# Kernel optimization log

Hardware: AMD Instinct MI355X
Metric: run time of the kernel (lower is better)

Reference implementation:

```python
import jax, jax.numpy as jnp
import numpy as np

B, N, P = 256, 32, 32
OBS, ACT = 96, 32
OBS_P, ACT_P = 96, 32
DIN = OBS + ACT          # obs_act_input_dim = 128
DOUT = 128               # obs_act_output_dim
DIN_P = OBS_P + ACT_P    # obs_act_input_dim_people = 128
DOUT_P = 128             # obs_act_output_dim_people
DF1, DF2 = 64, 32        # final hidden / final_output_dim


def setup_inputs() -> dict:
    key = jax.random.key(0)
    ks = jax.random.split(key, 13)
    s = 0.05
    return {
        "states": jax.random.normal(ks[0], (B, N, OBS), jnp.float32),
        "policies": jax.random.uniform(ks[1], (B, N, ACT), jnp.float32),
        "actions": jax.random.uniform(ks[2], (B, N, ACT), jnp.float32),
        "states_people": jax.random.normal(ks[3], (B, P, OBS_P), jnp.float32),
        "actions_people": jax.random.uniform(ks[4], (B, P, ACT_P), jnp.float32),
        "W_k": jax.random.normal(ks[5], (DIN, DOUT), jnp.float32) * s,
        "W_q": jax.random.normal(ks[6], (DIN, DOUT), jnp.float32) * s,
        "W_v": jax.random.normal(ks[7], (DIN, DOUT), jnp.float32) * s,
        "W_kp": jax.random.normal(ks[8], (DIN_P, DOUT_P), jnp.float32) * s,
        "W_qp": jax.random.normal(ks[9], (DIN, DOUT), jnp.float32) * s,
        "W_vp": jax.random.normal(ks[10], (DIN_P, DOUT_P), jnp.float32) * s,
        "W_f1": jax.random.normal(ks[11], (DOUT + DOUT_P, DF1), jnp.float32) * s,
        "W_f2": jax.random.normal(ks[12], (DF1, DF2), jnp.float32) * s,
    }


def reference(states, policies, actions, states_people, actions_people,
              W_k, W_q, W_v, W_kp, W_qp, W_vp, W_f1, W_f2):
    n = states.shape[1]
    p = states_people.shape[1]
    dk = jnp.asarray(W_k.shape[1], states.dtype)
    dkp = jnp.asarray(W_kp.shape[1], states.dtype)

    oa = jnp.concatenate([states, actions], axis=-1)    # [B,N,DIN]
    op = jnp.concatenate([states, policies], axis=-1)   # [B,N,DIN]

    k = oa @ W_k   # [B,N,DOUT]
    q = oa @ W_q   # [B,N,DOUT]
    scores = jnp.einsum('bid,bjd->bij', q, k)            # [B,N,N]
    # torch path: transpose then softmax over last axis of transposed scores
    weight = jax.nn.softmax(jnp.swapaxes(scores, 1, 2) / jnp.sqrt(dk), axis=-1)  # [B,N,N]

    # place_policies/place_actions masks == identity selector over (i==j)
    eye = jnp.eye(n, dtype=oa.dtype)[None, :, :, None]   # [1,N,N,1]
    oap = eye * op[:, None, :, :] + (1.0 - eye) * oa[:, None, :, :]  # [B,N,N,DIN]
    av = jnp.tanh(oap @ W_v)                             # [B,N,N,DOUT]
    # torch: mean_j( av[b,i,j] * weight[b,a,j] ) -> [B,N(a),N(i),DOUT]
    wav = jnp.einsum('baj,bijd->baid', weight, av) / n

    oa_p = jnp.concatenate([states_people, actions_people], axis=-1)  # [B,P,DIN_P]
    kp = oa_p @ W_kp                                     # [B,P,DOUT_P]
    qp = oa @ W_qp                                       # [B,N,DOUT_P]
    avp = jnp.tanh(oa_p @ W_vp)                          # [B,P,DOUT_P]
    scores_p = jnp.einsum('bnd,bpd->bnp', qp, kp)        # [B,N,P]
    # original softmax over dim=-2 (agents)
    wp = jax.nn.softmax(scores_p / jnp.sqrt(dkp), axis=-2)           # [B,N,P]
    wavp = jnp.einsum('bnp,bpd->bnd', wp, avp) / p       # mean over people

    wavp_b = jnp.broadcast_to(wavp[:, :, None, :], wav.shape[:3] + (wavp.shape[-1],))
    node_features = jnp.concatenate([wav, wavp_b], axis=-1)          # [B,N,N,256]

    h = jax.nn.leaky_relu(node_features @ W_f1)          # slope 0.01 (torch default)
    value = h @ W_f2                                     # [B,N,N,DF2]
    return value, weight, wp[..., None]
```

## Files before the change

kernel.cpp:

```cpp
#include <hip/hip_runtime.h>

#define VAL_SZ  (256*32*32*32)
#define W_OFF   VAL_SZ
#define WP_OFF  (VAL_SZ + 256*32*32)

#define PK_WV   0
#define PK_WVP  16384
#define PK_WQ   32768
#define PK_WK   49152
#define PK_WQP  65536
#define PK_WKP  81920
#define PK_WF1  98304
#define PK_WF2  114688

typedef short  bf16x8 __attribute__((ext_vector_type(8)));
typedef float  f32x4  __attribute__((ext_vector_type(4)));

#define MFMA(a, b, c) __builtin_amdgcn_mfma_f32_16x16x32_bf16(a, b, c, 0, 0, 0)

static __device__ __forceinline__ unsigned short f2bf(float f) {
    union { float f; unsigned u; } v; v.f = f;
    unsigned r = (v.u + 0x7FFF + ((v.u >> 16) & 1)) >> 16;
    return (unsigned short)r;
}
static __device__ __forceinline__ float bf2f(unsigned short u) {
    union { unsigned u; float f; } v; v.u = ((unsigned)u) << 16;
    return v.f;
}
static __device__ __forceinline__ float fast_tanh(float x) {
    x = fminf(fmaxf(x, -12.0f), 12.0f);
    float e = __expf(2.0f * x);
    return (e - 1.0f) / (e + 1.0f);
}

static __device__ __forceinline__ bf16x8 afrag(const unsigned short* Mb, int stride,
                                               int row0, int kt) {
    int lane = threadIdx.x & 63;
    return *(const bf16x8*)(Mb + (row0 + (lane & 15)) * stride + kt * 32 + (lane >> 4) * 8);
}

static __device__ __forceinline__ bf16x8 bfrag_pk(const unsigned short* base, int NT,
                                                  int kt, int nt) {
    int lane = threadIdx.x & 63;
    return *(const bf16x8*)(base + (((kt * NT + nt) * 64) + lane) * 8);
}

__global__ __launch_bounds__(256) void pack_lite(
    const float* __restrict__ Wk, const float* __restrict__ Wq,
    const float* __restrict__ Wv, const float* __restrict__ Wkp,
    const float* __restrict__ Wqp, const float* __restrict__ Wvp,
    const float* __restrict__ Wf1, const float* __restrict__ Wf2,
    unsigned short* __restrict__ pk)
{
    const float scale = 0.08838834764831845f;
    int gid = blockIdx.x * 256 + threadIdx.x;
    if (gid >= 14592) return;

    const float* W; int off, NT, ldn; float s = 1.0f;
    int r;
    if (gid < 12288) {
        int mat = gid >> 11;
        r = gid & 2047;
        NT = 8; ldn = 128;
        switch (mat) {
            case 0: W = Wv;  off = PK_WV;  break;
            case 1: W = Wvp; off = PK_WVP; break;
            case 2: W = Wq;  off = PK_WQ;  s = scale; break;
            case 3: W = Wk;  off = PK_WK;  break;
            case 4: W = Wqp; off = PK_WQP; s = scale; break;
            default: W = Wkp; off = PK_WKP; break;
        }
    } else if (gid < 14336) {
        r = gid - 12288; W = Wf1; off = PK_WF1; NT = 4; ldn = 64;
    } else {
        r = gid - 14336; W = Wf2; off = PK_WF2; NT = 2; ldn = 32;
    }
    int lane = r & 63;
    int l16 = lane & 15, quad = lane >> 4;
    int ktnt = r >> 6;
    int nt = ktnt % NT, kt = ktnt / NT;
    int n = nt * 16 + l16;
    int kb = kt * 32 + quad * 8;
    union { unsigned short u[8]; bf16x8 v; } o;
#pragma unroll
    for (int j = 0; j < 8; ++j) o.u[j] = f2bf(W[(kb + j) * ldn + n] * s);
    *(bf16x8*)(pk + off + (ktnt * 64 + lane) * 8) = o.v;
}

__global__ __launch_bounds__(1024) void critic_fused(
    const float* __restrict__ states, const float* __restrict__ policies,
    const float* __restrict__ actions, const float* __restrict__ states_p,
    const float* __restrict__ actions_p,
    const unsigned short* __restrict__ pk, float* __restrict__ out)
{
    __shared__ __align__(16) unsigned char SM[64000];
    unsigned short* OA  = (unsigned short*)(SM + 0);
    unsigned short* TD  = (unsigned short*)(SM + 8704);
    unsigned short* NF  = (unsigned short*)(SM + 0);
    unsigned short* OP  = (unsigned short*)(SM + 17408);
    unsigned short* QL  = (unsigned short*)(SM + 26112);
    unsigned short* WPB = (unsigned short*)(SM + 26112);
    float*          FP  = (float*)(SM + 26112);
    unsigned short* KL  = (unsigned short*)(SM + 34816);
    float*          GP  = (float*)(SM + 34816);
    unsigned short* VT  = (unsigned short*)(SM + 43520);
    unsigned short* AVT = (unsigned short*)(SM + 51712);
    unsigned short* SB1 = (unsigned short*)(SM + 59904);
    unsigned short* SB2 = (unsigned short*)(SM + 61952);

    const int tid = threadIdx.x;
    const int b = blockIdx.x;
    const int lane = tid & 63, wv = tid >> 6;
    const int l16 = lane & 15, quad = lane >> 4;
    const float invN = 1.0f / 32.0f;
    const f32x4 Z = {0.f, 0.f, 0.f, 0.f};

    {
        const float* st = states   + (size_t)b * 3072;
        const float* ac = actions  + (size_t)b * 1024;
        const float* po = policies + (size_t)b * 1024;
#pragma unroll
        for (int k = 0; k < 4; ++k) {
            int idx = tid + k * 1024;
            int n = idx >> 7, d = idx & 127;
            float sv, pv;
            if (d < 96) { sv = st[n * 96 + d]; pv = sv; }
            else        { sv = ac[n * 32 + d - 96]; pv = po[n * 32 + d - 96]; }
            OA[n * 136 + d] = f2bf(sv);
            OP[n * 136 + d] = f2bf(pv);
        }
    }
    __syncthreads();

    if (wv < 8) {
        int mt = wv & 1, ntA = wv >> 1, ntB = ntA + 4;
        f32x4 va0 = Z, va1 = Z, vp0 = Z, vp1 = Z;
#pragma unroll
        for (int kt = 0; kt < 4; ++kt) {
            bf16x8 aA = afrag(OA, 136, mt * 16, kt);
            bf16x8 aP = afrag(OP, 136, mt * 16, kt);
            bf16x8 b0 = bfrag_pk(pk + PK_WV, 8, kt, ntA);
            bf16x8 b1 = bfrag_pk(pk + PK_WV, 8, kt, ntB);
            va0 = MFMA(aA, b0, va0); va1 = MFMA(aA, b1, va1);
            vp0 = MFMA(aP, b0, vp0); vp1 = MFMA(aP, b1, vp1);
        }
#pragma unroll
        for (int r = 0; r < 4; ++r) {
            int row = mt * 16 + quad * 4 + r;
            float tva0 = fast_tanh(va0[r]), tvp0 = fast_tanh(vp0[r]);
            float tva1 = fast_tanh(va1[r]), tvp1 = fast_tanh(vp1[r]);
            VT[(ntA * 16 + l16) * 32 + row] = f2bf(tva0);
            VT[(ntB * 16 + l16) * 32 + row] = f2bf(tva1);
            TD[row * 136 + ntA * 16 + l16] = f2bf(tvp0 - tva0);
            TD[row * 136 + ntB * 16 + l16] = f2bf(tvp1 - tva1);
        }
    } else {
        int s = wv - 8;
        int mt = s & 1, pb2 = s >> 1;
        bf16x8 afr[4];
#pragma unroll
        for (int kt = 0; kt < 4; ++kt) afr[kt] = afrag(OA, 136, mt * 16, kt);
#pragma unroll
        for (int m2 = 0; m2 < 2; ++m2) {
            const unsigned short* pkM = pk + (m2 ? PK_WK : PK_WQ);
            unsigned short* dst = m2 ? KL : QL;
#pragma unroll
            for (int h = 0; h < 2; ++h) {
                int nt = pb2 + h * 4;
                f32x4 acc = Z;
#pragma unroll
                for (int kt = 0; kt < 4; ++kt)
                    acc = MFMA(afr[kt], bfrag_pk(pkM, 8, kt, nt), acc);
#pragma unroll
                for (int r = 0; r < 4; ++r)
                    dst[(mt * 16 + quad * 4 + r) * 136 + nt * 16 + l16] = f2bf(acc[r]);
            }
        }
    }
    __syncthreads();

    f32x4 gReg = Z;
    int gmt = 0, gnt = 0;
    if (wv < 8) {
        gmt = wv & 1; gnt = wv >> 1;
#pragma unroll
        for (int kt = 0; kt < 4; ++kt)
            gReg = MFMA(afrag(TD, 136, gmt * 16, kt), bfrag_pk(pk + PK_WF1, 4, kt, gnt), gReg);
    } else if (wv < 12) {
        int s = wv - 8;
        int mt = s & 1, nt = s >> 1;
        f32x4 acc = Z;
#pragma unroll
        for (int kt = 0; kt < 4; ++kt)
            acc = MFMA(afrag(QL, 136, mt * 16, kt), afrag(KL, 136, nt * 16, kt), acc);
#pragma unroll
        for (int r = 0; r < 4; ++r)
            SB1[(nt * 16 + l16) * 32 + mt * 16 + quad * 4 + r] = f2bf(acc[r]);
    } else {
        const float* st = states_p  + (size_t)b * 3072;
        const float* ac = actions_p + (size_t)b * 1024;
        int t256 = tid - 768;
#pragma unroll
        for (int k = 0; k < 16; ++k) {
            int idx = t256 + k * 256;
            int n = idx >> 7, d = idx & 127;
            OP[n * 136 + d] = f2bf((d < 96) ? st[n * 96 + d] : ac[n * 32 + d - 96]);
        }
    }
    __syncthreads();

    {
        int mt = wv & 1, nt = wv >> 1;
        bf16x8 ao[4], ap[4];
#pragma unroll
        for (int kt = 0; kt < 4; ++kt) {
            ao[kt] = afrag(OA, 136, mt * 16, kt);
            ap[kt] = afrag(OP, 136, mt * 16, kt);
        }
        f32x4 aq = Z, akp = Z, aav = Z;
#pragma unroll
        for (int kt = 0; kt < 4; ++kt) {
            aq  = MFMA(ao[kt], bfrag_pk(pk + PK_WQP, 8, kt, nt), aq);
            akp = MFMA(ap[kt], bfrag_pk(pk + PK_WKP, 8, kt, nt), akp);
            aav = MFMA(ap[kt], bfrag_pk(pk + PK_WVP, 8, kt, nt), aav);
        }
#pragma unroll
        for (int r = 0; r < 4; ++r) {
            int row = mt * 16 + quad * 4 + r;
            QL[row * 136 + nt * 16 + l16] = f2bf(aq[r]);
            KL[row * 136 + nt * 16 + l16] = f2bf(akp[r]);
            AVT[(nt * 16 + l16) * 32 + row] = f2bf(fast_tanh(aav[r]));
        }
    }
    __syncthreads();

    if (wv < 4) {
        int mt = wv & 1, nt = wv >> 1;
        f32x4 acc = Z;
#pragma unroll
        for (int kt = 0; kt < 4; ++kt)
            acc = MFMA(afrag(QL, 136, mt * 16, kt), afrag(KL, 136, nt * 16, kt), acc);
#pragma unroll
        for (int r = 0; r < 4; ++r)
            SB2[(nt * 16 + l16) * 32 + mt * 16 + quad * 4 + r] = f2bf(acc[r]);
    } else if (wv >= 8) {
        int t512 = tid - 512;
#pragma unroll
        for (int rep = 0; rep < 2; ++rep) {
            int idx = t512 + rep * 512;
            int j = idx & 31, a = idx >> 5;
            float x = bf2f(SB1[a * 32 + j]);
            float m = x;
#pragma unroll
            for (int msk = 16; msk >= 1; msk >>= 1) m = fmaxf(m, __shfl_xor(m, msk));
            float e = __expf(x - m);
            float s = e;
#pragma unroll
            for (int msk = 16; msk >= 1; msk >>= 1) s += __shfl_xor(s, msk);
            float w = e / s;
            out[W_OFF + (size_t)b * 1024 + a * 32 + j] = w;
            SB1[a * 32 + j] = f2bf(w);
        }
    }
    __syncthreads();

    if (wv < 8) {
#pragma unroll
        for (int rep = 0; rep < 2; ++rep) {
            int idx = tid + rep * 512;
            int n = idx & 31, p = idx >> 5;
            float x = bf2f(SB2[p * 32 + n]);
            float m = x;
#pragma unroll
            for (int msk = 16; msk >= 1; msk >>= 1) m = fmaxf(m, __shfl_xor(m, msk));
            float e = __expf(x - m);
            float s = e;
#pragma unroll
            for (int msk = 16; msk >= 1; msk >>= 1) s += __shfl_xor(s, msk);
            float w2 = e / s;
            out[WP_OFF + (size_t)b * 1024 + n * 32 + p] = w2;
            WPB[n * 32 + p] = f2bf(w2);
        }
    } else {
        int s = wv - 8;
        int mt = s & 1, nt0 = s >> 1, nt1 = nt0 + 4;
        bf16x8 aw = afrag(SB1, 32, mt * 16, 0);
        f32x4 s0 = MFMA(aw, afrag(VT, 32, nt0 * 16, 0), Z);
        f32x4 s1 = MFMA(aw, afrag(VT, 32, nt1 * 16, 0), Z);
#pragma unroll
        for (int r = 0; r < 4; ++r) {
            int row = mt * 16 + quad * 4 + r;
            NF[row * 264 + nt0 * 16 + l16] = f2bf(s0[r] * invN);
            NF[row * 264 + nt1 * 16 + l16] = f2bf(s1[r] * invN);
        }
    }
    __syncthreads();

    {
        int mt = wv & 1, nt = wv >> 1;
        f32x4 acc = MFMA(afrag(WPB, 32, mt * 16, 0), afrag(AVT, 32, nt * 16, 0), Z);
#pragma unroll
        for (int r = 0; r < 4; ++r) {
            int row = mt * 16 + quad * 4 + r;
            NF[row * 264 + 128 + nt * 16 + l16] = f2bf(acc[r] * invN);
        }
    }
    __syncthreads();

    if (wv < 8) {
        int mt = wv & 1, nt = wv >> 1;
        f32x4 f = Z;
#pragma unroll
        for (int kt = 0; kt < 8; ++kt)
            f = MFMA(afrag(NF, 264, mt * 16, kt), bfrag_pk(pk + PK_WF1, 4, kt, nt), f);
#pragma unroll
        for (int r = 0; r < 4; ++r) {
            FP[(mt * 16 + quad * 4 + r) * 66 + nt * 16 + l16] = f[r];
            GP[(gmt * 16 + quad * 4 + r) * 67 + gnt * 16 + l16] = gReg[r];
        }
    }
    __syncthreads();

    {
        bf16x8 bw[2][2];
#pragma unroll
        for (int kt = 0; kt < 2; ++kt)
#pragma unroll
            for (int nt = 0; nt < 2; ++nt)
                bw[kt][nt] = bfrag_pk(pk + PK_WF2, 2, kt, nt);

#pragma unroll
        for (int t4 = 0; t4 < 4; ++t4) {
            int tile = wv + t4 * 16;
            int m0 = tile * 16;
            int a = m0 >> 5;
            int i = (m0 & 31) + l16;
            float w = bf2f(SB1[a * 32 + i]) * invN;
            const float* Fa = FP + a * 66;
            const float* Gi = GP + i * 67;
            f32x4 acc0 = Z, acc1 = Z;
#pragma unroll
            for (int kt = 0; kt < 2; ++kt) {
                union { unsigned short u[8]; bf16x8 v; } h;
                int dbase = kt * 32 + quad * 8;
#pragma unroll
                for (int j = 0; j < 8; ++j) {
                    float z = fmaf(w, Gi[dbase + j], Fa[dbase + j]);
                    z = fmaxf(z, 0.01f * z);
                    h.u[j] = f2bf(z);
                }
                acc0 = MFMA(h.v, bw[kt][0], acc0);
                acc1 = MFMA(h.v, bw[kt][1], acc1);
            }
            float* base = out + (size_t)b * 32768 + (size_t)m0 * 32;
#pragma unroll
            for (int r = 0; r < 4; ++r) {
                int row = quad * 4 + r;
                base[row * 32 + l16]      = acc0[r];
                base[row * 32 + 16 + l16] = acc1[r];
            }
        }
    }
}

extern "C" void kernel_launch(void* const* d_in, const int* in_sizes, int n_in,
                              void* d_out, int out_size, void* d_ws, size_t ws_size,
                              hipStream_t stream)
{
    const float* states    = (const float*)d_in[0];
    const float* policies  = (const float*)d_in[1];
    const float* actions   = (const float*)d_in[2];
    const float* states_p  = (const float*)d_in[3];
    const float* actions_p = (const float*)d_in[4];
    const float* Wk        = (const float*)d_in[5];
    const float* Wq        = (const float*)d_in[6];
    const float* Wv        = (const float*)d_in[7];
    const float* Wkp       = (const float*)d_in[8];
    const float* Wqp       = (const float*)d_in[9];
    const float* Wvp       = (const float*)d_in[10];
    const float* Wf1       = (const float*)d_in[11];
    const float* Wf2       = (const float*)d_in[12];
    float* out = (float*)d_out;
    unsigned short* pk = (unsigned short*)d_ws;

    pack_lite<<<57, 256, 0, stream>>>(Wk, Wq, Wv, Wkp, Wqp, Wvp, Wf1, Wf2, pk);
    critic_fused<<<256, 1024, 0, stream>>>(states, policies, actions,
                                           states_p, actions_p, pk, out);
}
```

Before: 109.0 us.

## Reassociate node-feature projection through W_f1 and pad small LDS tiles

Instead of building the 32x256 node-feature matrix and multiplying it by W_f1, the kernel first projects the tanh value rows (VA, AVP) through their halves of W_f1, then applies the attention weights to those 64-wide projections. This removes the NF staging buffer, one barrier stage and the K=256 GEMM, and spreads the W_f1 work across earlier phases. Small score/weight tiles now use a row stride of 40 to cut LDS bank conflicts. The extra bf16 rounding of the intermediate projections changes numerics slightly.

```diff
diff --git a/kernel.cpp b/kernel.cpp
--- a/kernel.cpp
+++ b/kernel.cpp
@@ -93,20 +93,21 @@
     const float* __restrict__ actions_p,
     const unsigned short* __restrict__ pk, float* __restrict__ out)
 {
-    __shared__ __align__(16) unsigned char SM[64000];
-    unsigned short* OA  = (unsigned short*)(SM + 0);
-    unsigned short* TD  = (unsigned short*)(SM + 8704);
-    unsigned short* NF  = (unsigned short*)(SM + 0);
-    unsigned short* OP  = (unsigned short*)(SM + 17408);
-    unsigned short* QL  = (unsigned short*)(SM + 26112);
-    unsigned short* WPB = (unsigned short*)(SM + 26112);
-    float*          FP  = (float*)(SM + 26112);
-    unsigned short* KL  = (unsigned short*)(SM + 34816);
-    float*          GP  = (float*)(SM + 34816);
-    unsigned short* VT  = (unsigned short*)(SM + 43520);
-    unsigned short* AVT = (unsigned short*)(SM + 51712);
-    unsigned short* SB1 = (unsigned short*)(SM + 59904);
-    unsigned short* SB2 = (unsigned short*)(SM + 61952);
+    __shared__ __align__(16) unsigned char SM[65024];
+    unsigned short* OA   = (unsigned short*)(SM + 0);
+    unsigned short* OP   = (unsigned short*)(SM + 8704);
+    unsigned short* TD   = (unsigned short*)(SM + 17408);
+    unsigned short* AVr  = (unsigned short*)(SM + 17408);
+    unsigned short* VAr  = (unsigned short*)(SM + 26112);
+    unsigned short* SB2  = (unsigned short*)(SM + 26112);
+    unsigned short* WPB  = (unsigned short*)(SM + 28672);
+    unsigned short* QL   = (unsigned short*)(SM + 34816);
+    float*          FP   = (float*)(SM + 34816);
+    unsigned short* KL   = (unsigned short*)(SM + 43520);
+    float*          GP   = (float*)(SM + 43520);
+    unsigned short* VA1T = (unsigned short*)(SM + 52224);
+    unsigned short* AV1T = (unsigned short*)(SM + 57344);
+    unsigned short* SB1  = (unsigned short*)(SM + 62464);
 
     const int tid = threadIdx.x;
     const int b = blockIdx.x;
@@ -149,8 +150,8 @@
             int row = mt * 16 + quad * 4 + r;
             float tva0 = fast_tanh(va0[r]), tvp0 = fast_tanh(vp0[r]);
             float tva1 = fast_tanh(va1[r]), tvp1 = fast_tanh(vp1[r]);
-            VT[(ntA * 16 + l16) * 32 + row] = f2bf(tva0);
-            VT[(ntB * 16 + l16) * 32 + row] = f2bf(tva1);
+            VAr[row * 136 + ntA * 16 + l16] = f2bf(tva0);
+            VAr[row * 136 + ntB * 16 + l16] = f2bf(tva1);
             TD[row * 136 + ntA * 16 + l16] = f2bf(tvp0 - tva0);
             TD[row * 136 + ntB * 16 + l16] = f2bf(tvp1 - tva1);
         }
@@ -183,9 +184,16 @@
     int gmt = 0, gnt = 0;
     if (wv < 8) {
         gmt = wv & 1; gnt = wv >> 1;
-#pragma unroll
-        for (int kt = 0; kt < 4; ++kt)
-            gReg = MFMA(afrag(TD, 136, gmt * 16, kt), bfrag_pk(pk + PK_WF1, 4, kt, gnt), gReg);
+        f32x4 v1 = Z;
+#pragma unroll
+        for (int kt = 0; kt < 4; ++kt) {
+            bf16x8 bw = bfrag_pk(pk + PK_WF1, 4, kt, gnt);
+            gReg = MFMA(afrag(TD, 136, gmt * 16, kt), bw, gReg);
+            v1   = MFMA(afrag(VAr, 136, gmt * 16, kt), bw, v1);
+        }
+#pragma unroll
+        for (int r = 0; r < 4; ++r)
+            VA1T[(gnt * 16 + l16) * 40 + gmt * 16 + quad * 4 + r] = f2bf(v1[r]);
     } else if (wv < 12) {
         int s = wv - 8;
         int mt = s & 1, nt = s >> 1;
@@ -195,7 +203,7 @@
             acc = MFMA(afrag(QL, 136, mt * 16, kt), afrag(KL, 136, nt * 16, kt), acc);
 #pragma unroll
         for (int r = 0; r < 4; ++r)
-            SB1[(nt * 16 + l16) * 32 + mt * 16 + quad * 4 + r] = f2bf(acc[r]);
+            SB1[(nt * 16 + l16) * 40 + mt * 16 + quad * 4 + r] = f2bf(acc[r]);
     } else {
         const float* st = states_p  + (size_t)b * 3072;
         const float* ac = actions_p + (size_t)b * 1024;
@@ -229,7 +237,7 @@
             int row = mt * 16 + quad * 4 + r;
             QL[row * 136 + nt * 16 + l16] = f2bf(aq[r]);
             KL[row * 136 + nt * 16 + l16] = f2bf(akp[r]);
-            AVT[(nt * 16 + l16) * 32 + row] = f2bf(fast_tanh(aav[r]));
+            AVr[row * 136 + nt * 16 + l16] = f2bf(fast_tanh(aav[r]));
         }
     }
     __syncthreads();
@@ -242,14 +250,25 @@
             acc = MFMA(afrag(QL, 136, mt * 16, kt), afrag(KL, 136, nt * 16, kt), acc);
 #pragma unroll
         for (int r = 0; r < 4; ++r)
-            SB2[(nt * 16 + l16) * 32 + mt * 16 + quad * 4 + r] = f2bf(acc[r]);
-    } else if (wv >= 8) {
-        int t512 = tid - 512;
-#pragma unroll
-        for (int rep = 0; rep < 2; ++rep) {
-            int idx = t512 + rep * 512;
+            SB2[(nt * 16 + l16) * 40 + mt * 16 + quad * 4 + r] = f2bf(acc[r]);
+    } else if (wv < 12) {
+        int s = wv - 4;
+        int amt = s & 1, ant = s >> 1;
+        f32x4 av1 = Z;
+#pragma unroll
+        for (int kt = 0; kt < 4; ++kt)
+            av1 = MFMA(afrag(AVr, 136, amt * 16, kt),
+                       bfrag_pk(pk + PK_WF1, 4, kt + 4, ant), av1);
+#pragma unroll
+        for (int r = 0; r < 4; ++r)
+            AV1T[(ant * 16 + l16) * 40 + amt * 16 + quad * 4 + r] = f2bf(av1[r]);
+    } else {
+        int t256 = tid - 768;
+#pragma unroll
+        for (int rep = 0; rep < 4; ++rep) {
+            int idx = t256 + rep * 256;
             int j = idx & 31, a = idx >> 5;
-            float x = bf2f(SB1[a * 32 + j]);
+            float x = bf2f(SB1[a * 40 + j]);
             float m = x;
 #pragma unroll
             for (int msk = 16; msk >= 1; msk >>= 1) m = fmaxf(m, __shfl_xor(m, msk));
@@ -259,17 +278,19 @@
             for (int msk = 16; msk >= 1; msk >>= 1) s += __shfl_xor(s, msk);
             float w = e / s;
             out[W_OFF + (size_t)b * 1024 + a * 32 + j] = w;
-            SB1[a * 32 + j] = f2bf(w);
-        }
-    }
-    __syncthreads();
-
-    if (wv < 8) {
-#pragma unroll
-        for (int rep = 0; rep < 2; ++rep) {
-            int idx = tid + rep * 512;
+            SB1[a * 40 + j] = f2bf(w);
+        }
+    }
+    __syncthreads();
+
+    f32x4 f1 = Z;
+    int fmt = 0, fnt = 0;
+    if (wv < 4) {
+#pragma unroll
+        for (int rep = 0; rep < 4; ++rep) {
+            int idx = tid + rep * 256;
             int n = idx & 31, p = idx >> 5;
-            float x = bf2f(SB2[p * 32 + n]);
+            float x = bf2f(SB2[p * 40 + n]);
             float m = x;
 #pragma unroll
             for (int msk = 16; msk >= 1; msk >>= 1) m = fmaxf(m, __shfl_xor(m, msk));
@@ -279,45 +300,24 @@
             for (int msk = 16; msk >= 1; msk >>= 1) s += __shfl_xor(s, msk);
             float w2 = e / s;
             out[WP_OFF + (size_t)b * 1024 + n * 32 + p] = w2;
-            WPB[n * 32 + p] = f2bf(w2);
-        }
-    } else {
+            WPB[n * 40 + p] = f2bf(w2);
+        }
+    } else if (wv >= 8) {
         int s = wv - 8;
-        int mt = s & 1, nt0 = s >> 1, nt1 = nt0 + 4;
-        bf16x8 aw = afrag(SB1, 32, mt * 16, 0);
-        f32x4 s0 = MFMA(aw, afrag(VT, 32, nt0 * 16, 0), Z);
-        f32x4 s1 = MFMA(aw, afrag(VT, 32, nt1 * 16, 0), Z);
-#pragma unroll
-        for (int r = 0; r < 4; ++r) {
-            int row = mt * 16 + quad * 4 + r;
-            NF[row * 264 + nt0 * 16 + l16] = f2bf(s0[r] * invN);
-            NF[row * 264 + nt1 * 16 + l16] = f2bf(s1[r] * invN);
-        }
-    }
-    __syncthreads();
-
-    {
-        int mt = wv & 1, nt = wv >> 1;
-        f32x4 acc = MFMA(afrag(WPB, 32, mt * 16, 0), afrag(AVT, 32, nt * 16, 0), Z);
-#pragma unroll
-        for (int r = 0; r < 4; ++r) {
-            int row = mt * 16 + quad * 4 + r;
-            NF[row * 264 + 128 + nt * 16 + l16] = f2bf(acc[r] * invN);
-        }
+        fmt = s & 1; fnt = s >> 1;
+        f1 = MFMA(afrag(SB1, 40, fmt * 16, 0), afrag(VA1T, 40, fnt * 16, 0), Z);
     }
     __syncthreads();
 
     if (wv < 8) {
-        int mt = wv & 1, nt = wv >> 1;
-        f32x4 f = Z;
-#pragma unroll
-        for (int kt = 0; kt < 8; ++kt)
-            f = MFMA(afrag(NF, 264, mt * 16, kt), bfrag_pk(pk + PK_WF1, 4, kt, nt), f);
-#pragma unroll
-        for (int r = 0; r < 4; ++r) {
-            FP[(mt * 16 + quad * 4 + r) * 66 + nt * 16 + l16] = f[r];
+#pragma unroll
+        for (int r = 0; r < 4; ++r)
             GP[(gmt * 16 + quad * 4 + r) * 67 + gnt * 16 + l16] = gReg[r];
-        }
+    } else {
+        f1 = MFMA(afrag(WPB, 40, fmt * 16, 0), afrag(AV1T, 40, fnt * 16, 0), f1);
+#pragma unroll
+        for (int r = 0; r < 4; ++r)
+            FP[(fmt * 16 + quad * 4 + r) * 66 + fnt * 16 + l16] = f1[r] * invN;
     }
     __syncthreads();
 
@@ -335,7 +335,7 @@
             int m0 = tile * 16;
             int a = m0 >> 5;
             int i = (m0 & 31) + l16;
-            float w = bf2f(SB1[a * 32 + i]) * invN;
+            float w = bf2f(SB1[a * 40 + i]) * invN;
             const float* Fa = FP + a * 66;
             const float* Gi = GP + i * 67;
             f32x4 acc0 = Z, acc1 = Z;
```

Result: slower. 112.5 us (+3.2%).
